# Kernel tuning notes

Measured on AMD Instinct MI355X. Metric: run time of the kernel, lower is better.

Reference implementation:

```python
import jax, jax.numpy as jnp
import numpy as np

EPS = 1e-5
HEADS = 4

def _conv(x, w, pad):
    return jax.lax.conv_general_dilated(x, w, (1, 1), [(pad, pad), (pad, pad)],
                                        dimension_numbers=('NCHW', 'OIHW', 'NCHW'))

def _gn(x, g, b, groups=8):
    B, C, H, W = x.shape
    xg = x.reshape(B, groups, C // groups, H, W)
    m = xg.mean((2, 3, 4), keepdims=True)
    v = xg.var((2, 3, 4), keepdims=True)
    xn = ((xg - m) * jax.lax.rsqrt(v + EPS)).reshape(B, C, H, W)
    return xn * g[None, :, None, None] + b[None, :, None, None]

def _bn(x, g, b):  # training-mode BatchNorm2d (batch statistics)
    m = x.mean((0, 2, 3), keepdims=True)
    v = x.var((0, 2, 3), keepdims=True)
    return (x - m) * jax.lax.rsqrt(v + EPS) * g[None, :, None, None] + b[None, :, None, None]

def _resize_ac(x, Ho, Wo):  # bilinear, align_corners=True
    B, C, H, W = x.shape
    if (H, W) == (Ho, Wo):
        return x
    ys = jnp.linspace(0.0, H - 1.0, Ho)
    xs = jnp.linspace(0.0, W - 1.0, Wo)
    y0 = jnp.floor(ys).astype(jnp.int32); y1 = jnp.minimum(y0 + 1, H - 1)
    x0 = jnp.floor(xs).astype(jnp.int32); x1 = jnp.minimum(x0 + 1, W - 1)
    wy = (ys - y0)[None, None, :, None]
    wx = (xs - x0)[None, None, None, :]
    rows = x[:, :, y0, :] * (1.0 - wy) + x[:, :, y1, :] * wy
    return rows[:, :, :, x0] * (1.0 - wx) + rows[:, :, :, x1] * wx

def _idwt_haar(ll, lh, hl, hh):  # single-level inverse haar, zero mode
    B, C, H, W = ll.shape
    x00 = (ll + lh + hl + hh) * 0.5
    x01 = (ll - lh + hl - hh) * 0.5
    x10 = (ll + lh - hl - hh) * 0.5
    x11 = (ll - lh - hl + hh) * 0.5
    r0 = jnp.stack([x00, x01], -1).reshape(B, C, H, 2 * W)
    r1 = jnp.stack([x10, x11], -1).reshape(B, C, H, 2 * W)
    return jnp.stack([r0, r1], 3).reshape(B, C, 2 * H, 2 * W)

def setup_inputs() -> dict:
    key = jax.random.key(0)
    ks = iter(jax.random.split(key, 16))
    def nrm(shape, s=0.05):
        return jax.random.normal(next(ks), shape, jnp.float32) * s
    B, Cin, Cd, H, W = 4, 256, 128, 64, 64
    A = 128  # attention_dim
    return {
        'x': nrm((B, Cin, H, W), 1.0),
        'skip_detail': nrm((B, Cd, H, W), 1.0),
        'skip_structure': nrm((B, Cd, 2 * H, 2 * W), 1.0),
        'skip_global': nrm((B, Cd, H, W), 1.0),
        'W_up': nrm((Cd, Cin, 3, 3)),
        'bn_up_g': jnp.ones(Cd), 'bn_up_b': jnp.zeros(Cd),
        'W_ll': nrm((Cd // 4, Cd, 3, 3)),
        'gn_ll_g': jnp.ones(Cd // 4), 'gn_ll_b': jnp.zeros(Cd // 4),
        'W_high': nrm((3 * Cd // 4, Cd, 3, 3)),
        'gn_high_g': jnp.ones(3 * Cd // 4), 'gn_high_b': jnp.zeros(3 * Cd // 4),
        'w_scale': jnp.float32(3.0),
        'W_adj': nrm((Cd, Cd // 4)),
        'gn_adj_g': jnp.ones(Cd), 'gn_adj_b': jnp.zeros(Cd),
        'Wq': nrm((3, A, Cd)), 'bq': jnp.zeros((3, A)),
        'Wk': nrm((3, A, Cd)), 'bk': jnp.zeros((3, A)),
        'Wv': nrm((3, A, Cd)), 'bv': jnp.zeros((3, A)),
        'W_fuse': nrm((Cd, 3 * A)), 'b_fuse': jnp.zeros(Cd),
        'gn_fuse_g': jnp.ones(Cd), 'gn_fuse_b': jnp.zeros(Cd),
        'gn_out_g': jnp.ones(Cd), 'gn_out_b': jnp.zeros(Cd),
        'W_r1': nrm((Cd, Cd, 3, 3)), 'bn1_g': jnp.ones(Cd), 'bn1_b': jnp.zeros(Cd),
        'W_r2': nrm((Cd, Cd, 3, 3)), 'bn2_g': jnp.ones(Cd), 'bn2_b': jnp.zeros(Cd),
    }

def reference(x, skip_detail, skip_structure, skip_global, W_up, bn_up_g, bn_up_b,
              W_ll, gn_ll_g, gn_ll_b, W_high, gn_high_g, gn_high_b, w_scale,
              W_adj, gn_adj_g, gn_adj_b, Wq, bq, Wk, bk, Wv, bv,
              W_fuse, b_fuse, gn_fuse_g, gn_fuse_b, gn_out_g, gn_out_b,
              W_r1, bn1_g, bn1_b, W_r2, bn2_g, bn2_b):
    B, _, H, W = x.shape
    Ho, Wo = 2 * H, 2 * W
    # --- WaveletReconstructUpsample on skip_detail (spatial matches x) ---
    sd = skip_detail.astype(jnp.float32)
    x_ll = jnp.tanh(_gn(_conv(sd, W_ll, 1), gn_ll_g, gn_ll_b, 8))
    x_hi = jnp.tanh(_gn(_conv(sd, W_high, 1), gn_high_g, gn_high_b, 8))
    scale = jnp.clip(w_scale, 1.0, 5.0)
    x_ll = x_ll * scale
    x_hi = x_hi * scale
    sub = x_ll.shape[1]
    lh, hl, hh = x_hi[:, :sub], x_hi[:, sub:2 * sub], x_hi[:, 2 * sub:]
    rec = _idwt_haar(x_ll, lh, hl, hh)  # (B, sub, Ho, Wo)
    skip_up = jax.nn.relu(_gn(jnp.einsum('oc,bchw->bohw', W_adj, rec), gn_adj_g, gn_adj_b, 8))
    xu = _resize_ac(x, Ho, Wo)
    xu = jax.nn.relu(_bn(_conv(xu, W_up, 1), bn_up_g, bn_up_b))
    merged = xu + skip_up  # (B, Cd, Ho, Wo)
    # --- tri-path multi-scale cross attention (channel attention, d x d) ---
    feats = jnp.stack([skip_up,
                       _resize_ac(skip_structure, Ho, Wo),
                       _resize_ac(skip_global, Ho, Wo)], 0)  # (3,B,C,Ho,Wo)
    A = Wq.shape[1]
    hd = A // HEADS
    N = Ho * Wo
    q = jnp.einsum('poc,bchw->pbohw', Wq, merged) + bq[:, None, :, None, None]
    k = jnp.einsum('poc,pbchw->pbohw', Wk, feats) + bk[:, None, :, None, None]
    v = jnp.einsum('poc,pbchw->pbohw', Wv, feats) + bv[:, None, :, None, None]
    q = q.reshape(3, B, HEADS, hd, N)
    k = k.reshape(3, B, HEADS, hd, N)
    v = v.reshape(3, B, HEADS, hd, N)
    attn = jnp.einsum('pbhdn,pbhen->pbhde', q.astype(jnp.float32), k.astype(jnp.float32))
    attn = jax.nn.softmax(attn / np.float32(np.sqrt(hd)), -1).astype(v.dtype)
    out = jnp.einsum('pbhde,pbhen->pbhdn', attn, v).reshape(3, B, A, Ho, Wo)
    tri = jnp.concatenate([out[0], out[1], out[2]], 1)  # (B, 3A, Ho, Wo)
    fused = jax.nn.silu(_gn(jnp.einsum('oc,bchw->bohw', W_fuse, tri)
                            + b_fuse[None, :, None, None], gn_fuse_g, gn_fuse_b, 8))
    att_out = _gn(merged + fused, gn_out_g, gn_out_b, 8)
    # --- refine conv (dropout is identity in eval / p handled as 0) ---
    r = jax.nn.relu(_bn(_conv(att_out, W_r1, 1), bn1_g, bn1_b))
    r = jax.nn.relu(_bn(_conv(r, W_r2, 1), bn2_g, bn2_b))
    return r
```

## Files before the change

kernel.cpp:

```cpp
#include <hip/hip_runtime.h>
#include <math.h>

#define EPSV 1e-5f

typedef __attribute__((ext_vector_type(8))) short short8;
typedef __attribute__((ext_vector_type(4))) float f32x4;

__device__ inline unsigned short f2bf(float x) {
  unsigned int u = __float_as_uint(x);
  return (unsigned short)((u + 0x7FFFu + ((u >> 16) & 1u)) >> 16);
}
__device__ inline float bf2f(unsigned short v) {
  return __uint_as_float(((unsigned int)v) << 16);
}

__global__ void packall_k(const float* __restrict__ W_up, const float* __restrict__ W_r1,
                          const float* __restrict__ W_r2, const float* __restrict__ W_ll,
                          const float* __restrict__ W_hi, unsigned short* __restrict__ p_up,
                          unsigned short* __restrict__ p_r1, unsigned short* __restrict__ p_r2,
                          unsigned short* __restrict__ p_dt) {
  int idx = blockIdx.x * 256 + threadIdx.x;
  const float* src; unsigned short* dst; int Cin, co_off, local;
  if (idx < 294912)       { src = W_up; dst = p_up; Cin = 256; co_off = 0;  local = idx; }
  else if (idx < 442368)  { src = W_r1; dst = p_r1; Cin = 128; co_off = 0;  local = idx - 294912; }
  else if (idx < 589824)  { src = W_r2; dst = p_r2; Cin = 128; co_off = 0;  local = idx - 442368; }
  else if (idx < 626688)  { src = W_ll; dst = p_dt; Cin = 128; co_off = 0;  local = idx - 589824; }
  else if (idx < 737280)  { src = W_hi; dst = p_dt; Cin = 128; co_off = 32; local = idx - 626688; }
  else return;
  int kk = local % 9;
  int ci = (local / 9) % Cin;
  int co = local / (9 * Cin);
  dst[((long)kk * 128 + co_off + co) * Cin + ci] = f2bf(src[local]);
}

__global__ void t_nhwc_k(const float* __restrict__ in, unsigned short* __restrict__ out,
                         unsigned short* __restrict__ out_nchw, int C, int HW) {
  __shared__ unsigned short lds[64][34];
  int b = blockIdx.z;
  int c0 = blockIdx.y << 5;
  int hw0 = blockIdx.x << 6;
  int t = threadIdx.x;
  int c = t >> 3, j0 = (t & 7) << 3;
  long ibase = ((long)b * C + c0 + c) * HW + hw0 + j0;
  const float* p = in + ibase;
  int4 nv; unsigned short* ns = (unsigned short*)&nv;
#pragma unroll
  for (int j = 0; j < 8; j++) {
    unsigned short v = f2bf(p[j]);
    lds[j0 + j][c] = v;
    ns[j] = v;
  }
  if (out_nchw) *(int4*)(out_nchw + ibase) = nv;
  __syncthreads();
  int hw = t >> 2, k = (t & 3) << 3;
  unsigned short* q = out + ((long)(b * HW + hw0 + hw)) * C + c0 + k;
  int4 val;
  unsigned short* vs = (unsigned short*)&val;
#pragma unroll
  for (int i = 0; i < 8; i++) vs[i] = lds[hw][k + i];
  *(int4*)q = val;
}

__global__ void gnout_nhwc_k(const float* __restrict__ in, const float* __restrict__ sums,
                             const float* __restrict__ gamma, const float* __restrict__ beta,
                             unsigned short* __restrict__ out) {
  __shared__ unsigned short lds[64][34];
  int b = blockIdx.z;
  int c0 = blockIdx.y << 5;
  int hw0 = blockIdx.x << 6;
  int t = threadIdx.x;
  int c = t >> 3, j0 = (t & 7) << 3;
  int ch = c0 + c;
  int sidx = b * 8 + (ch >> 4);
  const float ic = 1.f / 262144.f;
  float m = sums[2 * sidx] * ic;
  float r = rsqrtf(fmaxf(sums[2 * sidx + 1] * ic - m * m, 0.f) + EPSV);
  float ga = gamma[ch] * r, be = beta[ch] - m * r * gamma[ch];
  const float* p = in + (((long)(b * 128 + ch)) << 14) + hw0 + j0;
#pragma unroll
  for (int j = 0; j < 8; j++) lds[j0 + j][c] = f2bf(p[j] * ga + be);
  __syncthreads();
  int hw = t >> 2, k = (t & 3) << 3;
  unsigned short* q = out + ((long)(b * 16384 + hw0 + hw)) * 128 + c0 + k;
  int4 val;
  unsigned short* vs = (unsigned short*)&val;
#pragma unroll
  for (int i = 0; i < 8; i++) vs[i] = lds[hw][k + i];
  *(int4*)q = val;
}

__global__ void bnrelu_nhwc_k(const float* __restrict__ in, const float* __restrict__ sums,
                              const float* __restrict__ gamma, const float* __restrict__ beta,
                              unsigned short* __restrict__ out) {
  __shared__ unsigned short lds[64][34];
  int b = blockIdx.z;
  int c0 = blockIdx.y << 5;
  int hw0 = blockIdx.x << 6;
  int t = threadIdx.x;
  int c = t >> 3, j0 = (t & 7) << 3;
  int ch = c0 + c;
  const float ic = 1.f / 65536.f;
  float m = sums[2 * ch] * ic;
  float r = rsqrtf(fmaxf(sums[2 * ch + 1] * ic - m * m, 0.f) + EPSV);
  float ga = gamma[ch] * r, be = beta[ch] - m * r * gamma[ch];
  const float* p = in + (((long)(b * 128 + ch)) << 14) + hw0 + j0;
#pragma unroll
  for (int j = 0; j < 8; j++) lds[j0 + j][c] = f2bf(fmaxf(p[j] * ga + be, 0.f));
  __syncthreads();
  int hw = t >> 2, k = (t & 3) << 3;
  unsigned short* q = out + ((long)(b * 16384 + hw0 + hw)) * 128 + c0 + k;
  int4 val;
  unsigned short* vs = (unsigned short*)&val;
#pragma unroll
  for (int i = 0; i < 8; i++) vs[i] = lds[hw][k + i];
  *(int4*)q = val;
}

__global__ __launch_bounds__(256) void resize_t_k(const float* __restrict__ in,
                                                  unsigned short* __restrict__ out,
                                                  int C, float s) {
  __shared__ float rows[2][32][68];
  int ho = blockIdx.x, cb = blockIdx.y, b = blockIdx.z;
  int t = threadIdx.x;
  float ys = ho * s;
  int y0 = (int)ys; float wy = ys - y0;
  int y1 = min(y0 + 1, 63);
  for (int i = t; i < 1024; i += 256) {
    int r = i >> 9, c = (i >> 4) & 31, seg = i & 15;
    const float* p = in + (((long)(b * C + cb * 32 + c)) << 12) + ((r ? y1 : y0) << 6) + (seg << 2);
    *(float4*)&rows[r][c][seg << 2] = *(const float4*)p;
  }
  __syncthreads();
  int cs = t & 3;
#pragma unroll
  for (int half = 0; half < 2; half++) {
    int wo = (t >> 2) + half * 64;
    float xs = wo * s;
    int x0 = (int)xs; float wx = xs - x0;
    int x1 = min(x0 + 1, 63);
    int4 val; unsigned short* vs = (unsigned short*)&val;
#pragma unroll
    for (int j = 0; j < 8; j++) {
      int c = cs * 8 + j;
      float v00 = rows[0][c][x0], v01 = rows[0][c][x1];
      float v10 = rows[1][c][x0], v11 = rows[1][c][x1];
      float r0 = v00 + (v01 - v00) * wx;
      float r1 = v10 + (v11 - v10) * wx;
      vs[j] = f2bf(r0 + (r1 - r0) * wy);
    }
    *(int4*)(out + ((long)((b * 128 + ho) * 128 + wo)) * C + cb * 32 + cs * 8) = val;
  }
}

__global__ void resize_nchwbf_k(const float* __restrict__ in, unsigned short* __restrict__ out,
                                float s) {
  long idx = (long)blockIdx.x * 256 + threadIdx.x;
  int seg = (int)(idx & 15); long t2 = idx >> 4;
  int ho = (int)(t2 & 127); t2 >>= 7;
  int c = (int)(t2 & 127); int b = (int)(t2 >> 7);
  float ys = ho * s;
  int y0 = (int)ys; float wy = ys - y0;
  int y1 = min(y0 + 1, 63);
  const float* p = in + (((long)(b * 128 + c)) << 12);
  int4 val; unsigned short* vs = (unsigned short*)&val;
#pragma unroll
  for (int j = 0; j < 8; j++) {
    int wo = seg * 8 + j;
    float xs = wo * s;
    int x0 = (int)xs; float wx = xs - x0;
    int x1 = min(x0 + 1, 63);
    float v00 = p[(y0 << 6) + x0], v01 = p[(y0 << 6) + x1];
    float v10 = p[(y1 << 6) + x0], v11 = p[(y1 << 6) + x1];
    float r0 = v00 + (v01 - v00) * wx;
    float r1 = v10 + (v11 - v10) * wx;
    vs[j] = f2bf(r0 + (r1 - r0) * wy);
  }
  *(int4*)(out + (((long)(b * 128 + c)) << 14) + (ho << 7) + seg * 8) = val;
}

template <int W_, int CIN, int COB, int FC, int FN>
__global__ __launch_bounds__(256) void conv2_k(
    const unsigned short* __restrict__ xin, const unsigned short* __restrict__ wpk,
    float* __restrict__ out, int H) {
  constexpr int CP = 40;
  __shared__ unsigned short wbuf[3 * COB * CP];
  __shared__ unsigned short rbuf[(W_ + 2) * CP];
  int h = blockIdx.x, b = blockIdx.y, cb = blockIdx.z;
  int t = threadIdx.x;
  int wid = t >> 6, lane = t & 63;
  int co0 = (wid >> 1) * (FC * 16);
  int n0 = (wid & 1) * (FN * 16);
  int lm = lane & 15, lk = lane >> 4;
  f32x4 acc[FC][FN];
#pragma unroll
  for (int i = 0; i < FC; i++)
#pragma unroll
    for (int j = 0; j < FN; j++) acc[i][j] = (f32x4){0.f, 0.f, 0.f, 0.f};

  constexpr int WEL = 3 * COB * 32 / 8;
  constexpr int REL = (W_ + 2) * 32 / 8;

  for (int c0 = 0; c0 < CIN; c0 += 32) {
    for (int ky = 0; ky < 3; ky++) {
      int hr = h + ky - 1;
      __syncthreads();
      for (int i = t; i < WEL + REL; i += 256) {
        if (i < WEL) {
          int e = i * 8;
          int kx = e / (COB * 32);
          int rem = e - kx * (COB * 32);
          int co = rem >> 5, ci = rem & 31;
          const unsigned short* g =
              wpk + ((long)((ky * 3 + kx) * 128 + cb * COB + co)) * CIN + c0 + ci;
          *(int4*)&wbuf[(kx * COB + co) * CP + ci] = *(const int4*)g;
        } else {
          int e = (i - WEL) * 8;
          int col = e >> 5, ci = e & 31;
          int gc = col - 1;
          int4 v = {0, 0, 0, 0};
          if (hr >= 0 && hr < H && gc >= 0 && gc < W_)
            v = *(const int4*)(xin + ((long)((b * H + hr) * W_ + gc)) * CIN + c0 + ci);
          *(int4*)&rbuf[col * CP + ci] = v;
        }
      }
      __syncthreads();
#pragma unroll
      for (int kx = 0; kx < 3; kx++) {
        short8 afr[FC], bfr[FN];
#pragma unroll
        for (int i = 0; i < FC; i++)
          afr[i] = *(const short8*)&wbuf[(kx * COB + co0 + i * 16 + lm) * CP + lk * 8];
#pragma unroll
        for (int j = 0; j < FN; j++)
          bfr[j] = *(const short8*)&rbuf[(n0 + j * 16 + lm + kx) * CP + lk * 8];
#pragma unroll
        for (int i = 0; i < FC; i++)
#pragma unroll
          for (int j = 0; j < FN; j++)
            acc[i][j] = __builtin_amdgcn_mfma_f32_16x16x32_bf16(afr[i], bfr[j], acc[i][j], 0, 0, 0);
      }
    }
  }
#pragma unroll
  for (int i = 0; i < FC; i++) {
#pragma unroll
    for (int r = 0; r < 4; r++) {
      int col = cb * COB + co0 + i * 16 + lk * 4 + r;
      long obase = (((long)(b * 128 + col)) * H + h) * W_;
#pragma unroll
      for (int j = 0; j < FN; j++)
        out[obase + n0 + j * 16 + lm] = acc[i][j][r];
    }
  }
}

template <int W_, int CIN, int COB, int FC, int FN>
__global__ __launch_bounds__(256) void conv3_k(
    const unsigned short* __restrict__ xin, const unsigned short* __restrict__ wpk,
    float* __restrict__ out, int H) {
  constexpr int CP = 40;
  __shared__ unsigned short rbuf[3 * (W_ + 2) * CP];
  int h = blockIdx.x, b = blockIdx.y, cb = blockIdx.z;
  int t = threadIdx.x;
  int wid = t >> 6, lane = t & 63;
  int co0 = cb * COB + (wid >> 1) * (FC * 16);
  int n0 = (wid & 1) * (FN * 16);
  int lm = lane & 15, lk = lane >> 4;
  f32x4 acc[FC][FN];
#pragma unroll
  for (int i = 0; i < FC; i++)
#pragma unroll
    for (int j = 0; j < FN; j++) acc[i][j] = (f32x4){0.f, 0.f, 0.f, 0.f};

  constexpr int RW = W_ + 2;
  constexpr int REL = 3 * RW * 32 / 8;

  for (int c0 = 0; c0 < CIN; c0 += 32) {
    short8 afr[9][FC];
#pragma unroll
    for (int kk = 0; kk < 9; kk++)
#pragma unroll
      for (int i = 0; i < FC; i++)
        afr[kk][i] = *(const short8*)(wpk +
            ((long)(kk * 128 + co0 + i * 16 + lm)) * CIN + c0 + lk * 8);
    __syncthreads();
    for (int i = t; i < REL; i += 256) {
      int r = i / (RW * 4);
      int rem = i - r * (RW * 4);
      int col = rem >> 2, q = rem & 3;
      int hr = h + r - 1, gc = col - 1;
      int4 v = {0, 0, 0, 0};
      if (hr >= 0 && hr < H && gc >= 0 && gc < W_)
        v = *(const int4*)(xin + ((long)((b * H + hr) * W_ + gc)) * CIN + c0 + q * 8);
      *(int4*)&rbuf[(r * RW + col) * CP + q * 8] = v;
    }
    __syncthreads();
#pragma unroll
    for (int ky = 0; ky < 3; ky++) {
#pragma unroll
      for (int kx = 0; kx < 3; kx++) {
        short8 bfr[FN];
#pragma unroll
        for (int j = 0; j < FN; j++)
          bfr[j] = *(const short8*)&rbuf[(ky * RW + n0 + j * 16 + lm + kx) * CP + lk * 8];
#pragma unroll
        for (int i = 0; i < FC; i++)
#pragma unroll
          for (int j = 0; j < FN; j++)
            acc[i][j] = __builtin_amdgcn_mfma_f32_16x16x32_bf16(afr[ky * 3 + kx][i], bfr[j],
                                                                acc[i][j], 0, 0, 0);
      }
    }
  }
#pragma unroll
  for (int i = 0; i < FC; i++) {
#pragma unroll
    for (int r = 0; r < 4; r++) {
      int col = co0 + i * 16 + lk * 4 + r;
      long obase = (((long)(b * 128 + col)) * H + h) * W_;
#pragma unroll
      for (int j = 0; j < FN; j++)
        out[obase + n0 + j * 16 + lm] = acc[i][j][r];
    }
  }
}

__global__ void gn_sums_k(const float* __restrict__ x, float* __restrict__ sums,
                          int Ctot, int coff, int cpg, int HW, int goff) {
  int bg = blockIdx.x; int b = bg >> 3, g = bg & 7;
  const float* p = x + ((long)b * Ctot + coff + (long)g * cpg) * HW;
  long len = (long)cpg * HW;
  long chunk = len / gridDim.y;
  long s = (long)blockIdx.y * chunk, e = s + chunk;
  float s0 = 0.f, s1 = 0.f;
  for (long i = s + threadIdx.x; i < e; i += 256) {
    float v = p[i]; s0 += v; s1 += v * v;
  }
  __shared__ float r0[256], r1[256];
  int t = threadIdx.x;
  r0[t] = s0; r1[t] = s1;
  __syncthreads();
  for (int off = 128; off > 0; off >>= 1) {
    if (t < off) { r0[t] += r0[t + off]; r1[t] += r1[t + off]; }
    __syncthreads();
  }
  if (t == 0) {
    int gi = b * 16 + goff + g;
    atomicAdd(&sums[2 * gi], r0[0]);
    atomicAdd(&sums[2 * gi + 1], r1[0]);
  }
}

__global__ void bn_sums_k(const float* __restrict__ x, float* __restrict__ sums, int C) {
  int c = blockIdx.x;
  long total = 4L << 14;
  long chunk = total / gridDim.y;
  long s = (long)blockIdx.y * chunk, e = s + chunk;
  float s0 = 0.f, s1 = 0.f;
  for (long i = s + threadIdx.x; i < e; i += 256) {
    int b = (int)(i >> 14); int hw = (int)(i & 16383);
    float v = x[(((long)b * C + c) << 14) + hw];
    s0 += v; s1 += v * v;
  }
  __shared__ float r0[256], r1[256];
  int t = threadIdx.x;
  r0[t] = s0; r1[t] = s1;
  __syncthreads();
  for (int off = 128; off > 0; off >>= 1) {
    if (t < off) { r0[t] += r0[t + off]; r1[t] += r1[t + off]; }
    __syncthreads();
  }
  if (t == 0) { atomicAdd(&sums[2 * c], r0[0]); atomicAdd(&sums[2 * c + 1], r1[0]); }
}

__global__ void idwt_k(const float* __restrict__ det, const float* __restrict__ sd,
                       const float* __restrict__ gll, const float* __restrict__ bll,
                       const float* __restrict__ ghi, const float* __restrict__ bhi,
                       const float* __restrict__ wsc, float* __restrict__ rec) {
  long idx = ((long)blockIdx.x << 8) + threadIdx.x;
  if (idx >= (long)4 * 32 * 64 * 64) return;
  int j = (int)(idx & 63); long t = idx >> 6;
  int i = (int)(t & 63); t >>= 6;
  int c = (int)(t & 31); int b = (int)(t >> 5);
  float s = wsc[0]; s = fminf(fmaxf(s, 1.f), 5.f);
  const float icll = 1.f / 16384.f, ichi = 1.f / 49152.f;
  const float* dp = det + ((long)b << 19);
  long sp = ((long)i << 6) + j;
  int gi = b * 16 + (c >> 2);
  float m = sd[2 * gi] * icll;
  float r = rsqrtf(fmaxf(sd[2 * gi + 1] * icll - m * m, 0.f) + EPSV);
  float ll = tanhf((dp[((long)c << 12) + sp] - m) * r * gll[c] + bll[c]) * s;
  int hc = c; gi = b * 16 + 8 + hc / 12;
  m = sd[2 * gi] * ichi; r = rsqrtf(fmaxf(sd[2 * gi + 1] * ichi - m * m, 0.f) + EPSV);
  float lh = tanhf((dp[((long)(32 + hc) << 12) + sp] - m) * r * ghi[hc] + bhi[hc]) * s;
  hc = 32 + c; gi = b * 16 + 8 + hc / 12;
  m = sd[2 * gi] * ichi; r = rsqrtf(fmaxf(sd[2 * gi + 1] * ichi - m * m, 0.f) + EPSV);
  float hl = tanhf((dp[((long)(32 + hc) << 12) + sp] - m) * r * ghi[hc] + bhi[hc]) * s;
  hc = 64 + c; gi = b * 16 + 8 + hc / 12;
  m = sd[2 * gi] * ichi; r = rsqrtf(fmaxf(sd[2 * gi + 1] * ichi - m * m, 0.f) + EPSV);
  float hh = tanhf((dp[((long)(32 + hc) << 12) + sp] - m) * r * ghi[hc] + bhi[hc]) * s;
  float x00 = (ll + lh + hl + hh) * 0.5f;
  float x01 = (ll - lh + hl - hh) * 0.5f;
  float x10 = (ll + lh - hl - hh) * 0.5f;
  float x11 = (ll - lh - hl + hh) * 0.5f;
  float* rp = rec + (((long)b * 32 + c) << 14) + ((long)i << 8) + (j << 1);
  rp[0] = x00; rp[1] = x01; rp[128] = x10; rp[129] = x11;
}

__global__ __launch_bounds__(256) void adj_k(const float* __restrict__ rec,
                                             const float* __restrict__ Wadj,
                                             float* __restrict__ out,
                                             float* __restrict__ gsums) {
  __shared__ float ls[32][256];
  int n0 = blockIdx.x << 8;
  int o0 = blockIdx.y << 4;
  int b = blockIdx.z;
  int t = threadIdx.x;
  for (int idx = t; idx < 32 * 256; idx += 256) {
    int c = idx >> 8, n = idx & 255;
    ls[c][n] = rec[(((long)b * 32 + c) << 14) + n0 + n];
  }
  __syncthreads();
  float acc[16];
#pragma unroll
  for (int i = 0; i < 16; i++) acc[i] = 0.f;
  for (int c = 0; c < 32; c++) {
    float v = ls[c][t];
#pragma unroll
    for (int i = 0; i < 16; i++) acc[i] += v * Wadj[(o0 + i) * 32 + c];
  }
  float s0 = 0.f, s1 = 0.f;
#pragma unroll
  for (int i = 0; i < 16; i++) {
    out[(((long)b * 128 + o0 + i) << 14) + n0 + t] = acc[i];
    s0 += acc[i]; s1 += acc[i] * acc[i];
  }
  __syncthreads();
  float* red = (float*)ls;
  red[t] = s0; red[256 + t] = s1;
  __syncthreads();
  for (int off = 128; off > 0; off >>= 1) {
    if (t < off) { red[t] += red[t + off]; red[256 + t] += red[256 + t + off]; }
    __syncthreads();
  }
  if (t == 0) {
    int gi = b * 8 + (o0 >> 4);
    atomicAdd(&gsums[2 * gi], red[0]);
    atomicAdd(&gsums[2 * gi + 1], red[256]);
  }
}

__global__ void gn_relu_k(float* __restrict__ x, const float* __restrict__ sums,
                          const float* __restrict__ gamma, const float* __restrict__ beta) {
  long i0 = ((long)blockIdx.x * 256 + threadIdx.x) * 8;
  int ch = (int)((i0 >> 14) & 127);
  int b = (int)(i0 >> 21);
  int sidx = b * 8 + (ch >> 4);
  const float ic = 1.f / 262144.f;
  float m = sums[2 * sidx] * ic;
  float r = rsqrtf(fmaxf(sums[2 * sidx + 1] * ic - m * m, 0.f) + EPSV);
  float ga = gamma[ch] * r, be = beta[ch] - m * r * gamma[ch];
#pragma unroll
  for (int j = 0; j < 8; j++) {
    float v = fmaxf(x[i0 + j] * ga + be, 0.f);
    x[i0 + j] = v;
  }
}

__global__ void bn_apply8_k(float* __restrict__ x, const float* __restrict__ sums,
                            const float* __restrict__ gamma, const float* __restrict__ beta,
                            const float* __restrict__ add, unsigned short* __restrict__ obf) {
  long i0 = ((long)blockIdx.x * 256 + threadIdx.x) * 8;
  int ch = (int)((i0 >> 14) & 127);
  const float ic = 1.f / 65536.f;
  float m = sums[2 * ch] * ic;
  float r = rsqrtf(fmaxf(sums[2 * ch + 1] * ic - m * m, 0.f) + EPSV);
  float ga = gamma[ch] * r, be = beta[ch] - m * r * gamma[ch];
  int4 ov; unsigned short* os = (unsigned short*)&ov;
#pragma unroll
  for (int j = 0; j < 8; j++) {
    float v = fmaxf(x[i0 + j] * ga + be, 0.f);
    if (add) v += add[i0 + j];
    x[i0 + j] = v;
    os[j] = f2bf(v);
  }
  if (obf) *(int4*)(obf + i0) = ov;
}

__global__ void gn_silu_add_k(float* __restrict__ x, const float* __restrict__ sums,
                              const float* __restrict__ gamma, const float* __restrict__ beta,
                              const float* __restrict__ add, float* __restrict__ osums) {
  long i0 = ((long)blockIdx.x * 256 + threadIdx.x) * 8;
  int ch = (int)((i0 >> 14) & 127);
  int b = (int)(i0 >> 21);
  int sidx = b * 8 + (ch >> 4);
  const float ic = 1.f / 262144.f;
  float m = sums[2 * sidx] * ic;
  float r = rsqrtf(fmaxf(sums[2 * sidx + 1] * ic - m * m, 0.f) + EPSV);
  float ga = gamma[ch] * r, be = beta[ch] - m * r * gamma[ch];
  float s0 = 0.f, s1 = 0.f;
#pragma unroll
  for (int j = 0; j < 8; j++) {
    float v = x[i0 + j] * ga + be;
    v = v / (1.f + expf(-v));
    v += add[i0 + j];
    x[i0 + j] = v;
    s0 += v; s1 += v * v;
  }
  __shared__ float r0[256], r1[256];
  int t = threadIdx.x;
  r0[t] = s0; r1[t] = s1;
  __syncthreads();
  for (int off = 128; off > 0; off >>= 1) {
    if (t < off) { r0[t] += r0[t + off]; r1[t] += r1[t + off]; }
    __syncthreads();
  }
  if (t == 0) {
    atomicAdd(&osums[2 * sidx], r0[0]);
    atomicAdd(&osums[2 * sidx + 1], r1[0]);
  }
}

__global__ void colsum4_k(const unsigned short* __restrict__ m, const unsigned short* __restrict__ f0,
                          const unsigned short* __restrict__ f1, const unsigned short* __restrict__ f2,
                          float* __restrict__ S) {
  int bc = blockIdx.x, which = blockIdx.y;
  const unsigned short* p = (which == 0 ? m : which == 1 ? f0 : which == 2 ? f1 : f2) + ((long)bc << 14);
  float a = 0.f;
  for (int i = threadIdx.x; i < 2048; i += 256) {
    int4 v = *(const int4*)(p + i * 8);
    unsigned short* vs = (unsigned short*)&v;
#pragma unroll
    for (int j = 0; j < 8; j++) a += bf2f(vs[j]);
  }
  __shared__ float red[256];
  red[threadIdx.x] = a;
  __syncthreads();
  for (int off = 128; off > 0; off >>= 1) {
    if (threadIdx.x < off) red[threadIdx.x] += red[threadIdx.x + off];
    __syncthreads();
  }
  if (threadIdx.x == 0) S[which * 512 + bc] = red[0];
}

__global__ __launch_bounds__(256) void gram_mfma_k(
    const unsigned short* __restrict__ mbf, const unsigned short* __restrict__ f0,
    const unsigned short* __restrict__ f1, const unsigned short* __restrict__ f2,
    float* __restrict__ Gpart) {
  constexpr int CP = 40;
  __shared__ unsigned short As[128 * CP], Bs[128 * CP];
  int nc = blockIdx.x, p = blockIdx.y, b = blockIdx.z;
  const unsigned short* fp = (p == 0 ? f0 : p == 1 ? f1 : f2);
  const unsigned short* ma = mbf + ((long)b << 21);
  const unsigned short* fa = fp + ((long)b << 21);
  int t = threadIdx.x;
  int wid = t >> 6, lane = t & 63;
  int c0 = (wid >> 1) << 6;
  int cp0 = (wid & 1) << 6;
  int lm = lane & 15, lk = lane >> 4;
  f32x4 acc[4][4];
#pragma unroll
  for (int i = 0; i < 4; i++)
#pragma unroll
    for (int j = 0; j < 4; j++) acc[i][j] = (f32x4){0.f, 0.f, 0.f, 0.f};
  for (int ks = 0; ks < 16; ks++) {
    int n = (nc << 9) + (ks << 5);
    __syncthreads();
#pragma unroll
    for (int i = 0; i < 2; i++) {
      int idx = t + (i << 8);
      int row = idx >> 2, q = idx & 3;
      *(int4*)&As[row * CP + q * 8] = *(const int4*)(ma + ((long)row << 14) + n + q * 8);
      *(int4*)&Bs[row * CP + q * 8] = *(const int4*)(fa + ((long)row << 14) + n + q * 8);
    }
    __syncthreads();
    short8 af[4], bfr[4];
#pragma unroll
    for (int i = 0; i < 4; i++) af[i] = *(const short8*)&As[(c0 + i * 16 + lm) * CP + lk * 8];
#pragma unroll
    for (int j = 0; j < 4; j++) bfr[j] = *(const short8*)&Bs[(cp0 + j * 16 + lm) * CP + lk * 8];
#pragma unroll
    for (int i = 0; i < 4; i++)
#pragma unroll
      for (int j = 0; j < 4; j++)
        acc[i][j] = __builtin_amdgcn_mfma_f32_16x16x32_bf16(af[i], bfr[j], acc[i][j], 0, 0, 0);
  }
  float* Gp = Gpart + (((long)(nc * 12 + p * 4 + b)) << 14);
#pragma unroll
  for (int i = 0; i < 4; i++)
#pragma unroll
    for (int j = 0; j < 4; j++) {
      int cp = cp0 + j * 16 + lm;
#pragma unroll
      for (int r = 0; r < 4; r++) {
        int c = c0 + i * 16 + lk * 4 + r;
        Gp[c * 128 + cp] = acc[i][j][r];
      }
    }
}

__global__ void gred_k(const float* __restrict__ Gpart, float* __restrict__ G) {
  int cell = blockIdx.x * 256 + threadIdx.x;
  int pb = cell >> 14, rem = cell & 16383;
  float a = 0.f;
  for (int nc = 0; nc < 32; nc++) a += Gpart[(((long)(nc * 12 + pb)) << 14) + rem];
  G[cell] = a;
}

__global__ __launch_bounds__(256) void attn_k(const float* __restrict__ G,
                                              const float* __restrict__ Sall,
                                              const float* __restrict__ Wq,
                                              const float* __restrict__ bq,
                                              const float* __restrict__ Wk,
                                              const float* __restrict__ bk,
                                              float* __restrict__ attn) {
  int h = blockIdx.x, b = blockIdx.y, p = blockIdx.z;
  __shared__ float T[32][129];
  __shared__ float QS2[32], KS1[32];
  __shared__ float L[32][33];
  const float* S2 = Sall;
  const float* S1 = Sall + 512;
  const float* Gpb = G + ((long)(p * 4 + b) << 14);
  const float* Wqp = Wq + p * 16384;
  const float* Wkp = Wk + p * 16384;
  int t = threadIdx.x;
  if (t < 32) {
    float a = 0.f;
    for (int c = 0; c < 128; c++) a += Wqp[(h * 32 + t) * 128 + c] * S2[b * 128 + c];
    QS2[t] = a;
  } else if (t < 64) {
    int e = t - 32;
    float a = 0.f;
    for (int c = 0; c < 128; c++) a += Wkp[(h * 32 + e) * 128 + c] * S1[(p * 4 + b) * 128 + c];
    KS1[e] = a;
  }
  __syncthreads();
  for (int ii = t; ii < 4096; ii += 256) {
    int d = ii >> 7, cp = ii & 127;
    float a = 0.f;
    for (int c = 0; c < 128; c++) a += Wqp[(h * 32 + d) * 128 + c] * Gpb[c * 128 + cp];
    T[d][cp] = a;
  }
  __syncthreads();
  const float scale = 0.17677669529663687f;
  for (int ii = t; ii < 1024; ii += 256) {
    int d = ii >> 5, e = ii & 31;
    float a = 0.f;
    for (int cp = 0; cp < 128; cp++) a += T[d][cp] * Wkp[(h * 32 + e) * 128 + cp];
    float bqv = bq[p * 128 + h * 32 + d], bkv = bk[p * 128 + h * 32 + e];
    a += bqv * KS1[e] + bkv * QS2[d] + 16384.f * bqv * bkv;
    L[d][e] = a * scale;
  }
  __syncthreads();
  if (t < 32) {
    float mx = -1e30f;
    for (int e = 0; e < 32; e++) mx = fmaxf(mx, L[t][e]);
    float sum = 0.f;
    for (int e = 0; e < 32; e++) { float ev = expf(L[t][e] - mx); L[t][e] = ev; sum += ev; }
    float inv = 1.f / sum;
    float* ap = attn + ((((long)(p * 4 + b)) * 4 + h) * 32 + t) * 32;
    for (int e = 0; e < 32; e++) ap[e] = L[t][e] * inv;
  }
}

__global__ void m_k(const float* __restrict__ Wf, const float* __restrict__ attn,
                    const float* __restrict__ bv, float* __restrict__ M,
                    float* __restrict__ cbias) {
  int o = blockIdx.x, b = blockIdx.y, p = blockIdx.z;
  int ap = threadIdx.x;
  int h = ap >> 5;
  const float* at = attn + (((long)(p * 4 + b)) * 4 + h) * 1024;
  const float* wrow = Wf + o * 384 + p * 128 + h * 32;
  int e = ap & 31;
  float acc = 0.f;
  for (int d = 0; d < 32; d++) acc += wrow[d] * at[d * 32 + e];
  M[(((long)(p * 4 + b)) * 128 + o) * 128 + ap] = acc;
  __shared__ float red[128];
  red[ap] = acc * bv[p * 128 + ap];
  __syncthreads();
  for (int off = 64; off > 0; off >>= 1) {
    if (ap < off) red[ap] += red[ap + off];
    __syncthreads();
  }
  if (ap == 0) atomicAdd(&cbias[b * 128 + o], red[0]);
}

__global__ void weff_k(const float* __restrict__ M, const float* __restrict__ Wv,
                       unsigned short* __restrict__ Weff) {
  int o = blockIdx.x, b = blockIdx.y, p = blockIdx.z, c = threadIdx.x;
  const float* mrow = M + (((long)(p * 4 + b)) * 128 + o) * 128;
  const float* wv = Wv + p * 16384;
  float acc = 0.f;
  for (int a = 0; a < 128; a++) acc += mrow[a] * wv[a * 128 + c];
  Weff[((long)(b * 128 + o)) * 384 + p * 128 + c] = f2bf(acc);
}

__global__ __launch_bounds__(256) void fuse_mfma_k(
    const unsigned short* __restrict__ Wef, const unsigned short* __restrict__ f0t,
    const unsigned short* __restrict__ f1t, const unsigned short* __restrict__ f2t,
    const float* __restrict__ bf_, const float* __restrict__ cbias,
    float* __restrict__ out, float* __restrict__ gsums) {
  constexpr int CP = 40;
  __shared__ unsigned short As[64 * CP], Bs[128 * CP];
  __shared__ float sred[8];
  int nc = blockIdx.x, ob = blockIdx.y, b = blockIdx.z;
  int t = threadIdx.x;
  int wid = t >> 6, lane = t & 63;
  int o0 = (wid >> 1) * 32;
  int n0 = (wid & 1) * 64;
  int lm = lane & 15, lk = lane >> 4;
  if (t < 8) sred[t] = 0.f;
  f32x4 acc[2][4];
#pragma unroll
  for (int i = 0; i < 2; i++)
#pragma unroll
    for (int j = 0; j < 4; j++) acc[i][j] = (f32x4){0.f, 0.f, 0.f, 0.f};
  for (int kp = 0; kp < 12; kp++) {
    int k0 = kp << 5;
    int p = k0 >> 7, cc0 = k0 & 127;
    const unsigned short* ft = (p == 0 ? f0t : p == 1 ? f1t : f2t);
    __syncthreads();
    for (int i = t; i < 768; i += 256) {
      if (i < 256) {
        int row = i >> 2, q = i & 3;
        *(int4*)&As[row * CP + q * 8] =
            *(const int4*)(Wef + ((long)(b * 128 + ob * 64 + row)) * 384 + k0 + q * 8);
      } else {
        int j2 = i - 256;
        int n = j2 >> 2, q = j2 & 3;
        *(int4*)&Bs[n * CP + q * 8] =
            *(const int4*)(ft + ((long)(b * 16384 + nc * 128 + n)) * 128 + cc0 + q * 8);
      }
    }
    __syncthreads();
    short8 af[2], bfr[4];
#pragma unroll
    for (int i = 0; i < 2; i++) af[i] = *(const short8*)&As[(o0 + i * 16 + lm) * CP + lk * 8];
#pragma unroll
    for (int j = 0; j < 4; j++) bfr[j] = *(const short8*)&Bs[(n0 + j * 16 + lm) * CP + lk * 8];
#pragma unroll
    for (int i = 0; i < 2; i++)
#pragma unroll
      for (int j = 0; j < 4; j++)
        acc[i][j] = __builtin_amdgcn_mfma_f32_16x16x32_bf16(af[i], bfr[j], acc[i][j], 0, 0, 0);
  }
#pragma unroll
  for (int i = 0; i < 2; i++) {
    float s0 = 0.f, s1 = 0.f;
#pragma unroll
    for (int r = 0; r < 4; r++) {
      int o = ob * 64 + o0 + i * 16 + lk * 4 + r;
      float bias = bf_[o] + cbias[b * 128 + o];
#pragma unroll
      for (int j = 0; j < 4; j++) {
        int n = (nc << 7) + n0 + j * 16 + lm;
        float v = acc[i][j][r] + bias;
        out[(((long)(b * 128 + o)) << 14) + n] = v;
        s0 += v; s1 += v * v;
      }
    }
#pragma unroll
    for (int off = 1; off < 64; off <<= 1) {
      s0 += __shfl_xor(s0, off, 64);
      s1 += __shfl_xor(s1, off, 64);
    }
    if (lane == 0) {
      int gl = (o0 >> 4) + i;
      atomicAdd(&sred[2 * gl], s0);
      atomicAdd(&sred[2 * gl + 1], s1);
    }
  }
  __syncthreads();
  if (t < 8) {
    int g = b * 8 + ob * 4 + (t >> 1);
    atomicAdd(&gsums[2 * g + (t & 1)], sred[t]);
  }
}

extern "C" void kernel_launch(void* const* d_in, const int* in_sizes, int n_in,
                              void* d_out, int out_size, void* d_ws, size_t ws_size,
                              hipStream_t stream) {
  const float* x      = (const float*)d_in[0];
  const float* sdet   = (const float*)d_in[1];
  const float* sstru  = (const float*)d_in[2];
  const float* sglob  = (const float*)d_in[3];
  const float* W_up   = (const float*)d_in[4];
  const float* bnug   = (const float*)d_in[5];
  const float* bnub   = (const float*)d_in[6];
  const float* W_ll   = (const float*)d_in[7];
  const float* gllg   = (const float*)d_in[8];
  const float* gllb   = (const float*)d_in[9];
  const float* W_hi   = (const float*)d_in[10];
  const float* ghig   = (const float*)d_in[11];
  const float* ghib   = (const float*)d_in[12];
  const float* wsc    = (const float*)d_in[13];
  const float* W_adj  = (const float*)d_in[14];
  const float* gadjg  = (const float*)d_in[15];
  const float* gadjb  = (const float*)d_in[16];
  const float* Wq     = (const float*)d_in[17];
  const float* bq     = (const float*)d_in[18];
  const float* Wk     = (const float*)d_in[19];
  const float* bk     = (const float*)d_in[20];
  const float* Wv     = (const float*)d_in[21];
  const float* bv     = (const float*)d_in[22];
  const float* W_fu   = (const float*)d_in[23];
  const float* b_fu   = (const float*)d_in[24];
  const float* gfug   = (const float*)d_in[25];
  const float* gfub   = (const float*)d_in[26];
  const float* goug   = (const float*)d_in[27];
  const float* goub   = (const float*)d_in[28];
  const float* W_r1   = (const float*)d_in[29];
  const float* bn1g   = (const float*)d_in[30];
  const float* bn1b   = (const float*)d_in[31];
  const float* W_r2   = (const float*)d_in[32];
  const float* bn2g   = (const float*)d_in[33];
  const float* bn2b   = (const float*)d_in[34];
  float* out = (float*)d_out;

  float* ws = (float*)d_ws;
  size_t off = 0;
  auto alloc = [&](size_t n) { float* p = ws + off; off += n; return p; };
  float* bufA = alloc(8388608);
  float* det  = bufA;
  float* rec  = bufA + 2097152;
  float* Gpart = bufA;
  float* bufB = alloc(8388608);
  float* bufC = alloc(8388608);
  unsigned short* f1t = (unsigned short*)bufC;
  unsigned short* f2t = (unsigned short*)bufC + 8388608;
  unsigned short* xbf = (unsigned short*)alloc(8388608);
  unsigned short* f0t = (unsigned short*)alloc(4194304);
  unsigned short* mbf = (unsigned short*)alloc(4194304);
  unsigned short* f0  = (unsigned short*)alloc(4194304);
  unsigned short* f1  = (unsigned short*)alloc(4194304);
  unsigned short* f2  = (unsigned short*)alloc(4194304);
  float* Gm   = alloc(196608);
  unsigned short* wpk_up = (unsigned short*)alloc(147456);
  unsigned short* wpk_r1 = (unsigned short*)alloc(73728);
  unsigned short* wpk_r2 = (unsigned short*)alloc(73728);
  unsigned short* wpk_dt = (unsigned short*)alloc(36864);
  unsigned short* wefb   = (unsigned short*)alloc(98304);
  float* Sall = alloc(2048);
  float* attb = alloc(49152);
  float* Mb   = alloc(196608);
  float* zr = alloc(1600);
  float* cb      = zr;
  float* s_det   = zr + 512;
  float* s_adj   = zr + 640;
  float* s_bnup  = zr + 704;
  float* s_fuse  = zr + 960;
  float* s_gnout = zr + 1024;
  float* s_bn1   = zr + 1088;
  float* s_bn2   = zr + 1344;

  const float s63 = 63.f / 127.f;

  hipMemsetAsync(zr, 0, 1600 * sizeof(float), stream);
  packall_k<<<2880, 256, 0, stream>>>(W_up, W_r1, W_r2, W_ll, W_hi,
                                      wpk_up, wpk_r1, wpk_r2, wpk_dt);

  t_nhwc_k<<<dim3(64, 4, 4), 256, 0, stream>>>(sdet, xbf, nullptr, 128, 4096);
  conv2_k<64, 128, 32, 1, 2><<<dim3(64, 4, 4), 256, 0, stream>>>(xbf, wpk_dt, det, 64);
  gn_sums_k<<<dim3(32, 4), 256, 0, stream>>>(det, s_det, 128, 0, 4, 4096, 0);
  gn_sums_k<<<dim3(32, 8), 256, 0, stream>>>(det, s_det, 128, 32, 12, 4096, 8);
  idwt_k<<<2048, 256, 0, stream>>>(det, s_det, gllg, gllb, ghig, ghib, wsc, rec);

  adj_k<<<dim3(64, 8, 4), 256, 0, stream>>>(rec, W_adj, bufC, s_adj);
  gn_relu_k<<<4096, 256, 0, stream>>>(bufC, s_adj, gadjg, gadjb);

  resize_t_k<<<dim3(128, 8, 4), 256, 0, stream>>>(x, xbf, 256, s63);
  conv3_k<128, 256, 64, 2, 4><<<dim3(128, 4, 2), 256, 0, stream>>>(xbf, wpk_up, bufB, 128);
  bn_sums_k<<<dim3(128, 16), 256, 0, stream>>>(bufB, s_bnup, 128);
  bn_apply8_k<<<4096, 256, 0, stream>>>(bufB, s_bnup, bnug, bnub, bufC, mbf);

  t_nhwc_k<<<dim3(256, 4, 4), 256, 0, stream>>>(bufC, f0t, f0, 128, 16384);
  t_nhwc_k<<<dim3(256, 4, 4), 256, 0, stream>>>(sstru, f1t, f1, 128, 16384);
  resize_nchwbf_k<<<4096, 256, 0, stream>>>(sglob, f2, s63);
  resize_t_k<<<dim3(128, 4, 4), 256, 0, stream>>>(sglob, f2t, 128, s63);

  colsum4_k<<<dim3(512, 4), 256, 0, stream>>>(mbf, f0, f1, f2, Sall);
  gram_mfma_k<<<dim3(32, 3, 4), 256, 0, stream>>>(mbf, f0, f1, f2, Gpart);
  gred_k<<<768, 256, 0, stream>>>(Gpart, Gm);
  attn_k<<<dim3(4, 4, 3), 256, 0, stream>>>(Gm, Sall, Wq, bq, Wk, bk, attb);

  m_k<<<dim3(128, 4, 3), 128, 0, stream>>>(W_fu, attb, bv, Mb, cb);
  weff_k<<<dim3(128, 4, 3), 128, 0, stream>>>(Mb, Wv, wefb);
  fuse_mfma_k<<<dim3(128, 2, 4), 256, 0, stream>>>(wefb, f0t, f1t, f2t, b_fu, cb, bufA, s_fuse);

  gn_silu_add_k<<<4096, 256, 0, stream>>>(bufA, s_fuse, gfug, gfub, bufB, s_gnout);
  gnout_nhwc_k<<<dim3(256, 4, 4), 256, 0, stream>>>(bufA, s_gnout, goug, goub, xbf);

  conv3_k<128, 128, 64, 2, 4><<<dim3(128, 4, 2), 256, 0, stream>>>(xbf, wpk_r1, bufB, 128);
  bn_sums_k<<<dim3(128, 16), 256, 0, stream>>>(bufB, s_bn1, 128);
  bnrelu_nhwc_k<<<dim3(256, 4, 4), 256, 0, stream>>>(bufB, s_bn1, bn1g, bn1b, xbf);

  conv3_k<128, 128, 64, 2, 4><<<dim3(128, 4, 2), 256, 0, stream>>>(xbf, wpk_r2, out, 128);
  bn_sums_k<<<dim3(128, 16), 256, 0, stream>>>(out, s_bn2, 128);
  bn_apply8_k<<<4096, 256, 0, stream>>>(out, s_bn2, bn2g, bn2b, nullptr, nullptr);
}
```

Baseline: 943.6 us.

## Double-buffer weights and input row in LDS for the 3x3 conv

Replaces the 3x3 conv kernel with one that stages both the weight slice and a single input row per (channel chunk, ky) phase in shared memory. It double-buffers them, issuing global loads for the next phase into registers before the current MFMAs and storing them after. This is meant to hide global load latency and cut the per-thread register cost of holding nine weight fragments, and it leaves one barrier per phase instead of two. The price is more phases (three per channel chunk), a larger LDS footprint, and input rows reloaded per ky.

```diff
diff --git a/kernel.cpp b/kernel.cpp
--- a/kernel.cpp
+++ b/kernel.cpp
@@ -255,15 +255,24 @@
 }
 
 template <int W_, int CIN, int COB, int FC, int FN>
-__global__ __launch_bounds__(256) void conv3_k(
+__global__ __launch_bounds__(256) void conv4_k(
     const unsigned short* __restrict__ xin, const unsigned short* __restrict__ wpk,
     float* __restrict__ out, int H) {
   constexpr int CP = 40;
-  __shared__ unsigned short rbuf[3 * (W_ + 2) * CP];
+  constexpr int WROWS = 3 * COB;
+  constexpr int RROWS = W_ + 2;
+  constexpr int BUF = (WROWS + RROWS) * CP;
+  __shared__ unsigned short sbuf[2][BUF];
+  constexpr int WEL = WROWS * 32 / 8;
+  constexpr int REL = RROWS * 32 / 8;
+  constexpr int TOT = WEL + REL;
+  constexpr int NLD = (TOT + 255) / 256;
+  constexpr int NPH = (CIN / 32) * 3;
+
   int h = blockIdx.x, b = blockIdx.y, cb = blockIdx.z;
   int t = threadIdx.x;
   int wid = t >> 6, lane = t & 63;
-  int co0 = cb * COB + (wid >> 1) * (FC * 16);
+  int co0 = (wid >> 1) * (FC * 16);
   int n0 = (wid & 1) * (FN * 16);
   int lm = lane & 15, lk = lane >> 4;
   f32x4 acc[FC][FN];
@@ -272,51 +281,71 @@
 #pragma unroll
     for (int j = 0; j < FN; j++) acc[i][j] = (f32x4){0.f, 0.f, 0.f, 0.f};
 
-  constexpr int RW = W_ + 2;
-  constexpr int REL = 3 * RW * 32 / 8;
-
-  for (int c0 = 0; c0 < CIN; c0 += 32) {
-    short8 afr[9][FC];
-#pragma unroll
-    for (int kk = 0; kk < 9; kk++)
+  int4 v[NLD]; int dst[NLD];
+  auto load_phase = [&](int ph) {
+    int c3 = ph / 3;
+    int ky = ph - c3 * 3;
+    int c0 = c3 << 5;
+    int hr = h + ky - 1;
+#pragma unroll
+    for (int k = 0; k < NLD; k++) {
+      int i = t + k * 256;
+      int4 val = {0, 0, 0, 0};
+      int d = -1;
+      if (i < WEL) {
+        int e = i * 8;
+        int kx = e / (COB * 32);
+        int rem = e - kx * (COB * 32);
+        int co = rem >> 5, ci = rem & 31;
+        val = *(const int4*)(wpk + ((long)((ky * 3 + kx) * 128 + cb * COB + co)) * CIN + c0 + ci);
+        d = (kx * COB + co) * CP + ci;
+      } else if (i < TOT) {
+        int e = (i - WEL) * 8;
+        int col = e >> 5, ci = e & 31;
+        int gc = col - 1;
+        if (hr >= 0 && hr < H && gc >= 0 && gc < W_)
+          val = *(const int4*)(xin + ((long)((b * H + hr) * W_ + gc)) * CIN + c0 + ci);
+        d = (WROWS + col) * CP + ci;
+      }
+      v[k] = val; dst[k] = d;
+    }
+  };
+  auto store_phase = [&](int buf) {
+#pragma unroll
+    for (int k = 0; k < NLD; k++)
+      if (dst[k] >= 0) *(int4*)&sbuf[buf][dst[k]] = v[k];
+  };
+
+  load_phase(0);
+  store_phase(0);
+  __syncthreads();
+  for (int p = 0; p < NPH; p++) {
+    if (p + 1 < NPH) load_phase(p + 1);
+    const unsigned short* cw = sbuf[p & 1];
+    const unsigned short* cr = sbuf[p & 1] + WROWS * CP;
+#pragma unroll
+    for (int kx = 0; kx < 3; kx++) {
+      short8 afr[FC], bfr[FN];
 #pragma unroll
       for (int i = 0; i < FC; i++)
-        afr[kk][i] = *(const short8*)(wpk +
-            ((long)(kk * 128 + co0 + i * 16 + lm)) * CIN + c0 + lk * 8);
-    __syncthreads();
-    for (int i = t; i < REL; i += 256) {
-      int r = i / (RW * 4);
-      int rem = i - r * (RW * 4);
-      int col = rem >> 2, q = rem & 3;
-      int hr = h + r - 1, gc = col - 1;
-      int4 v = {0, 0, 0, 0};
-      if (hr >= 0 && hr < H && gc >= 0 && gc < W_)
-        v = *(const int4*)(xin + ((long)((b * H + hr) * W_ + gc)) * CIN + c0 + q * 8);
-      *(int4*)&rbuf[(r * RW + col) * CP + q * 8] = v;
-    }
-    __syncthreads();
-#pragma unroll
-    for (int ky = 0; ky < 3; ky++) {
-#pragma unroll
-      for (int kx = 0; kx < 3; kx++) {
-        short8 bfr[FN];
+        afr[i] = *(const short8*)&cw[(kx * COB + co0 + i * 16 + lm) * CP + lk * 8];
+#pragma unroll
+      for (int j = 0; j < FN; j++)
+        bfr[j] = *(const short8*)&cr[(n0 + j * 16 + lm + kx) * CP + lk * 8];
+#pragma unroll
+      for (int i = 0; i < FC; i++)
 #pragma unroll
         for (int j = 0; j < FN; j++)
-          bfr[j] = *(const short8*)&rbuf[(ky * RW + n0 + j * 16 + lm + kx) * CP + lk * 8];
-#pragma unroll
-        for (int i = 0; i < FC; i++)
-#pragma unroll
-          for (int j = 0; j < FN; j++)
-            acc[i][j] = __builtin_amdgcn_mfma_f32_16x16x32_bf16(afr[ky * 3 + kx][i], bfr[j],
-                                                                acc[i][j], 0, 0, 0);
-      }
-    }
+          acc[i][j] = __builtin_amdgcn_mfma_f32_16x16x32_bf16(afr[i], bfr[j], acc[i][j], 0, 0, 0);
+    }
+    if (p + 1 < NPH) store_phase((p + 1) & 1);
+    __syncthreads();
   }
 #pragma unroll
   for (int i = 0; i < FC; i++) {
 #pragma unroll
     for (int r = 0; r < 4; r++) {
-      int col = co0 + i * 16 + lk * 4 + r;
+      int col = cb * COB + co0 + i * 16 + lk * 4 + r;
       long obase = (((long)(b * 128 + col)) * H + h) * W_;
 #pragma unroll
       for (int j = 0; j < FN; j++)
@@ -869,7 +898,7 @@
   gn_relu_k<<<4096, 256, 0, stream>>>(bufC, s_adj, gadjg, gadjb);
 
   resize_t_k<<<dim3(128, 8, 4), 256, 0, stream>>>(x, xbf, 256, s63);
-  conv3_k<128, 256, 64, 2, 4><<<dim3(128, 4, 2), 256, 0, stream>>>(xbf, wpk_up, bufB, 128);
+  conv4_k<128, 256, 64, 2, 4><<<dim3(128, 4, 2), 256, 0, stream>>>(xbf, wpk_up, bufB, 128);
   bn_sums_k<<<dim3(128, 16), 256, 0, stream>>>(bufB, s_bnup, 128);
   bn_apply8_k<<<4096, 256, 0, stream>>>(bufB, s_bnup, bnug, bnub, bufC, mbf);
 
@@ -890,11 +919,11 @@
   gn_silu_add_k<<<4096, 256, 0, stream>>>(bufA, s_fuse, gfug, gfub, bufB, s_gnout);
   gnout_nhwc_k<<<dim3(256, 4, 4), 256, 0, stream>>>(bufA, s_gnout, goug, goub, xbf);
 
-  conv3_k<128, 128, 64, 2, 4><<<dim3(128, 4, 2), 256, 0, stream>>>(xbf, wpk_r1, bufB, 128);
+  conv4_k<128, 128, 64, 2, 4><<<dim3(128, 4, 2), 256, 0, stream>>>(xbf, wpk_r1, bufB, 128);
   bn_sums_k<<<dim3(128, 16), 256, 0, stream>>>(bufB, s_bn1, 128);
   bnrelu_nhwc_k<<<dim3(256, 4, 4), 256, 0, stream>>>(bufB, s_bn1, bn1g, bn1b, xbf);
 
-  conv3_k<128, 128, 64, 2, 4><<<dim3(128, 4, 2), 256, 0, stream>>>(xbf, wpk_r2, out, 128);
+  conv4_k<128, 128, 64, 2, 4><<<dim3(128, 4, 2), 256, 0, stream>>>(xbf, wpk_r2, out, 128);
   bn_sums_k<<<dim3(128, 16), 256, 0, stream>>>(out, s_bn2, 128);
   bn_apply8_k<<<4096, 256, 0, stream>>>(out, s_bn2, bn2g, bn2b, nullptr, nullptr);
 }
```

Result: faster. 849.0 us (-10.0%).
